# Kernel tuning notes

Hardware: AMD Instinct MI355X
Metric: run time of the kernel (lower is better)

## Reference

```python
import jax, jax.numpy as jnp
import numpy as np

E = 128      # embedding_dim
H = 64       # hidden_dim
B = 2048     # batch
L = 200      # history length
NEG = -1e30  # stand-in for -inf (avoids NaN for all-pad rows; same math when any key unmasked)


def setup_inputs() -> dict:
    key = jax.random.key(0)
    ks = jax.random.split(key, 10)
    s1 = 1.0 / np.sqrt(4 * E)
    s2 = 1.0 / np.sqrt(H)
    return {
        "query": jax.random.normal(ks[0], (B, E), jnp.float32),
        "keys": jax.random.normal(ks[1], (B, L, E), jnp.float32),
        "mask": jax.random.randint(ks[2], (B, L), 0, 2, jnp.int32),
        "W1": jax.random.uniform(ks[3], (4 * E, H), jnp.float32, -s1, s1),
        "b1": jax.random.uniform(ks[4], (H,), jnp.float32, -s1, s1),
        "W2": jax.random.uniform(ks[5], (H, H), jnp.float32, -s2, s2),
        "b2": jax.random.uniform(ks[6], (H,), jnp.float32, -s2, s2),
        "W3": jax.random.uniform(ks[7], (H, 1), jnp.float32, -s2, s2),
        "b3": jax.random.uniform(ks[8], (1,), jnp.float32, -s2, s2),
        "no_hist": jax.random.normal(ks[9], (E,), jnp.float32) * 0.001,
    }


def reference(query, keys, mask, W1, b1, W2, b2, W3, b3, no_hist):
    # q expanded over L, 4-way concat features: [q, k, q*k, q-k] -> (B, L, 4E)
    q = jnp.broadcast_to(query[:, None, :], keys.shape)
    attn_in = jnp.concatenate([q, keys, q * keys, q - keys], axis=-1)
    # 3-layer MLP scorer -> (B, L)
    h = jax.nn.relu(attn_in @ W1 + b1)
    h = jax.nn.relu(h @ W2 + b2)
    scores = (h @ W3 + b3)[..., 0]
    # masked softmax over L, then zero masked slots and renormalize
    m = mask.astype(scores.dtype)
    scores = jnp.where(m == 0, NEG, scores)
    attn = jax.nn.softmax(scores, axis=1) * m
    denom = jnp.sum(attn, axis=1, keepdims=True)
    attn = attn / (denom + 1e-12)
    # weighted sum of keys -> (B, E)
    user_interest = jnp.einsum("bl,ble->be", attn, keys)
    # rows with no history get the learned no-hist embedding
    all_pad = jnp.sum(m, axis=1) == 0  # (B,)
    user_interest = jnp.where(all_pad[:, None], no_hist[None, :], user_interest)
    return user_interest
```

## Files before the change

kernel.cpp:

```cpp
#include <hip/hip_runtime.h>


#define NB 2048
#define LE 128
#define LH 64
#define LL 200

typedef short bf16x8 __attribute__((ext_vector_type(8)));
typedef float f32x4 __attribute__((ext_vector_type(4)));

__device__ float g_BD[8192];
__device__ float g_Cq[8192];
__device__ float g_AD[8192];
__device__ short g_W2T[4096];

__device__ __forceinline__ short f2bf(float f) {
  unsigned u = __float_as_uint(f);
  u += 0x7fffu + ((u >> 16) & 1u);
  return (short)(u >> 16);
}

__device__ __forceinline__ unsigned cvtpk(float a, float b) {
  unsigned d;
  asm("v_cvt_pk_bf16_f32 %0, %1, %2" : "=v"(d) : "v"(a), "v"(b));
  return d;
}

__global__ void k0_prep(const float* __restrict__ W1, const float* __restrict__ W2) {
  int idx = blockIdx.x * 256 + threadIdx.x;
  if (idx < 8192) {
    int h = idx >> 7, e = idx & 127;
    g_BD[idx] = W1[(128 + e) * LH + h] - W1[(384 + e) * LH + h];
    g_Cq[idx] = W1[(256 + e) * LH + h];
    int e2 = idx >> 6, h2 = idx & 63;
    g_AD[idx] = W1[e2 * LH + h2] + W1[(384 + e2) * LH + h2];
    if (idx < 4096) {
      int c = idx >> 6, k = idx & 63;
      g_W2T[idx] = f2bf(W2[k * LH + c]);
    }
  }
}

struct __align__(16) SM {
  short flds1[16 * 64 * 8];
  short flds2[8 * 64 * 8];
  short h1[4][16 * 68];
  float scores[208];
  float q[128];
  float bias1[64];
  float b2s[64];
  float w3s[64];
  float red[16];
  float redf[512];
};

__global__ void __launch_bounds__(256, 4)
din_attn(const float* __restrict__ query, const float* __restrict__ keysg,
         const int* __restrict__ mask, const float* __restrict__ b1,
         const float* __restrict__ b2, const float* __restrict__ W3,
         const float* __restrict__ no_hist, float* __restrict__ out)
{
  __shared__ SM sm;
  const int b    = blockIdx.x;
  const int t    = threadIdx.x;
  const int lane = t & 63;
  const int wv   = t >> 6;
  const int col  = lane & 15;
  const int quad = lane >> 4;

  int my_mask = 0;
  if (t < LL) my_mask = mask[b * LL + t];
  if (t < LE) sm.q[t] = query[b * LE + t];
  if (t < LH) { sm.b2s[t] = b2[t]; sm.w3s[t] = W3[t]; }
  __syncthreads();

  #pragma unroll
  for (int i = 0; i < 4; ++i) {
    int idx = (t + 256 * i) * 8;
    int h = idx >> 7, e0 = idx & 127;
    float4 bd0 = *(const float4*)&g_BD[idx];
    float4 bd1 = *(const float4*)&g_BD[idx + 4];
    float4 c0  = *(const float4*)&g_Cq[idx];
    float4 c1  = *(const float4*)&g_Cq[idx + 4];
    int4 w;
    w.x = (int)cvtpk(bd0.x + sm.q[e0 + 0] * c0.x, bd0.y + sm.q[e0 + 1] * c0.y);
    w.y = (int)cvtpk(bd0.z + sm.q[e0 + 2] * c0.z, bd0.w + sm.q[e0 + 3] * c0.w);
    w.z = (int)cvtpk(bd1.x + sm.q[e0 + 4] * c1.x, bd1.y + sm.q[e0 + 5] * c1.y);
    w.w = (int)cvtpk(bd1.z + sm.q[e0 + 6] * c1.z, bd1.w + sm.q[e0 + 7] * c1.w);
    int n = h >> 4, cc = h & 15, kt = e0 >> 5, qd = (e0 >> 3) & 3;
    *(int4*)&sm.flds1[(((n * 4 + kt) * 64) + qd * 16 + cc) * 8] = w;
  }
  {
    int l = t & 63, f0 = t >> 6;
    #pragma unroll
    for (int ii = 0; ii < 2; ++ii) {
      int f = f0 + ii * 4;
      int n = f >> 1, k2 = f & 1;
      int cc = l & 15, qd = l >> 4;
      *(bf16x8*)&sm.flds2[(f * 64 + l) * 8] =
          *(const bf16x8*)&g_W2T[(n * 16 + cc) * 64 + k2 * 32 + qd * 8];
    }
  }
  {
    int h = lane;
    float acc = 0.f;
    #pragma unroll 8
    for (int e = wv * 32; e < wv * 32 + 32; ++e)
      acc = fmaf(sm.q[e], g_AD[e * LH + h], acc);
    float* biasp = (float*)&sm.h1[0][0];
    biasp[wv * 64 + h] = acc;
  }
  __syncthreads();

  if (t < LH) {
    const float* biasp = (const float*)&sm.h1[0][0];
    sm.bias1[t] = b1[t] + biasp[t] + biasp[64 + t] + biasp[128 + t] + biasp[192 + t];
  }
  __syncthreads();

  const float* kb = keysg + (size_t)b * LL * LE;
  short* h1w = &sm.h1[wv][0];
  const int mts[4] = {wv, wv + 4, wv + 8, 12};
  bf16x8 ka[4][4];

  auto load_tile = [&](bf16x8 (&a)[4], int mt) {
    int row = mt * 16 + col;
    row = row < LL ? row : LL - 1;
    const float* rp = kb + row * LE;
    #pragma unroll
    for (int kt = 0; kt < 4; ++kt) {
      float4 v0 = *(const float4*)&rp[kt * 32 + quad * 8];
      float4 v1 = *(const float4*)&rp[kt * 32 + quad * 8 + 4];
      int4 w;
      w.x = (int)cvtpk(v0.x, v0.y);
      w.y = (int)cvtpk(v0.z, v0.w);
      w.z = (int)cvtpk(v1.x, v1.y);
      w.w = (int)cvtpk(v1.z, v1.w);
      a[kt] = *(bf16x8*)&w;
    }
  };

  auto compute_tile = [&](const bf16x8 (&a)[4], int mt) {
    #pragma unroll
    for (int n = 0; n < 4; ++n) {
      f32x4 acc = {0.f, 0.f, 0.f, 0.f};
      #pragma unroll
      for (int kt = 0; kt < 4; ++kt) {
        bf16x8 wf = *(const bf16x8*)&sm.flds1[((n * 4 + kt) * 64 + lane) * 8];
        acc = __builtin_amdgcn_mfma_f32_16x16x32_bf16(wf, a[kt], acc, 0, 0, 0);
      }
      float4 bb = *(const float4*)&sm.bias1[n * 16 + quad * 4];
      int2 wr;
      wr.x = (int)cvtpk(fmaxf(acc[0] + bb.x, 0.f), fmaxf(acc[1] + bb.y, 0.f));
      wr.y = (int)cvtpk(fmaxf(acc[2] + bb.z, 0.f), fmaxf(acc[3] + bb.w, 0.f));
      *(int2*)&h1w[col * 68 + n * 16 + quad * 4] = wr;
    }
    bf16x8 a2[2];
    #pragma unroll
    for (int k2 = 0; k2 < 2; ++k2)
      a2[k2] = *(const bf16x8*)&h1w[col * 68 + k2 * 32 + quad * 8];
    float p[4] = {0.f, 0.f, 0.f, 0.f};
    #pragma unroll
    for (int n = 0; n < 4; ++n) {
      bf16x8 w20 = *(const bf16x8*)&sm.flds2[((n * 2 + 0) * 64 + lane) * 8];
      bf16x8 w21 = *(const bf16x8*)&sm.flds2[((n * 2 + 1) * 64 + lane) * 8];
      f32x4 c2 = {0.f, 0.f, 0.f, 0.f};
      c2 = __builtin_amdgcn_mfma_f32_16x16x32_bf16(a2[0], w20, c2, 0, 0, 0);
      c2 = __builtin_amdgcn_mfma_f32_16x16x32_bf16(a2[1], w21, c2, 0, 0, 0);
      float bb = sm.b2s[n * 16 + col];
      float w3 = sm.w3s[n * 16 + col];
      #pragma unroll
      for (int j = 0; j < 4; ++j)
        p[j] = fmaf(fmaxf(c2[j] + bb, 0.f), w3, p[j]);
    }
    {
      bool s8 = (col & 8) != 0;
      float k0 = s8 ? p[2] : p[0], d0 = s8 ? p[0] : p[2];
      float k1 = s8 ? p[3] : p[1], d1 = s8 ? p[1] : p[3];
      k0 += __shfl_xor(d0, 8);
      k1 += __shfl_xor(d1, 8);
      bool s4 = (col & 4) != 0;
      float u = s4 ? k1 : k0, du = s4 ? k0 : k1;
      u += __shfl_xor(du, 4);
      u += __shfl_xor(u, 2);
      u += __shfl_xor(u, 1);
      if ((col & 3) == 0) sm.scores[mt * 16 + quad * 4 + (col >> 2)] = u;
    }
  };

  load_tile(ka[0], mts[0]);
  load_tile(ka[1], mts[1]);
  compute_tile(ka[0], mts[0]);
  load_tile(ka[2], mts[2]);
  compute_tile(ka[1], mts[1]);
  if (wv == 0) load_tile(ka[3], 12);
  compute_tile(ka[2], mts[2]);
  if (wv == 0) compute_tile(ka[3], 12);
  __syncthreads();

  float sc = (t < LL) ? sm.scores[t] : -3.0e38f;
  float vmax = (my_mask != 0) ? sc : -3.0e38f;
  #pragma unroll
  for (int off = 1; off < 64; off <<= 1) vmax = fmaxf(vmax, __shfl_xor(vmax, off));
  if (lane == 0) sm.red[wv] = vmax;
  __syncthreads();
  float M = fmaxf(fmaxf(sm.red[0], sm.red[1]), fmaxf(sm.red[2], sm.red[3]));
  float ex = (t < LL && my_mask != 0) ? __expf(sc - M) : 0.f;
  float vsum = ex;
  #pragma unroll
  for (int off = 1; off < 64; off <<= 1) vsum += __shfl_xor(vsum, off);
  if (lane == 0) sm.red[4 + wv] = vsum;
  __syncthreads();
  float Z = sm.red[4] + sm.red[5] + sm.red[6] + sm.red[7];
  bool allpad = !(Z > 0.f);
  float rz = allpad ? 0.f : (1.f / Z);
  if (t < 208) sm.scores[t] = (t < LL) ? ex * rz : 0.f;
  __syncthreads();

  {
    const int nt = (wv == 0) ? 4 : 3;
    float v[32];
    #pragma unroll
    for (int k = 0; k < 32; ++k) v[k] = 0.f;
    #pragma unroll
    for (int i = 0; i < 4; ++i) {
      if (i < nt) {
        float aw = sm.scores[mts[i] * 16 + col];
        #pragma unroll
        for (int kt = 0; kt < 4; ++kt) {
          const int* kv = (const int*)&ka[i][kt];
          #pragma unroll
          for (int w = 0; w < 4; ++w) {
            unsigned u = (unsigned)kv[w];
            v[kt * 8 + 2 * w]     = fmaf(aw, __uint_as_float(u << 16), v[kt * 8 + 2 * w]);
            v[kt * 8 + 2 * w + 1] = fmaf(aw, __uint_as_float(u & 0xffff0000u), v[kt * 8 + 2 * w + 1]);
          }
        }
      }
    }
    #pragma unroll
    for (int step = 0; step < 4; ++step) {
      const int off  = 8 >> step;
      const int half = 16 >> step;
      bool sel = (col & off) != 0;
      #pragma unroll
      for (int k = 0; k < 16; ++k) {
        if (k < half) {
          float keep = sel ? v[k + half] : v[k];
          float send = sel ? v[k] : v[k + half];
          v[k] = keep + __shfl_xor(send, off);
        }
      }
    }
    int e0 = (col >> 2) * 32 + quad * 8 + ((col & 3) * 2);
    *(float2*)&sm.redf[wv * 128 + e0] = make_float2(v[0], v[1]);
    __syncthreads();
    if (t < LE) {
      float s = sm.redf[t] + sm.redf[128 + t] + sm.redf[256 + t] + sm.redf[384 + t];
      if (allpad) s = no_hist[t];
      out[b * LE + t] = s;
    }
  }
}

extern "C" void kernel_launch(void* const* d_in, const int* in_sizes, int n_in,
                              void* d_out, int out_size, void* d_ws, size_t ws_size,
                              hipStream_t stream) {
  (void)in_sizes; (void)n_in; (void)ws_size; (void)out_size; (void)d_ws;
  const float* query   = (const float*)d_in[0];
  const float* keysg   = (const float*)d_in[1];
  const int*   mask    = (const int*)d_in[2];
  const float* W1      = (const float*)d_in[3];
  const float* b1      = (const float*)d_in[4];
  const float* W2      = (const float*)d_in[5];
  const float* b2      = (const float*)d_in[6];
  const float* W3      = (const float*)d_in[7];
  const float* no_hist = (const float*)d_in[9];

  k0_prep<<<32, 256, 0, stream>>>(W1, W2);
  din_attn<<<NB, 256, 0, stream>>>(query, keysg, mask, b1, b2, W3, no_hist,
                                   (float*)d_out);
}
```

Before: 313.5 us.

## Process two batch rows per block and prefetch first key tile early

The kernel now launches 1024 blocks that each loop over two batch rows, so per-block setup (W2 fragment staging, b2/W3 loads) is amortized. For each row, the first key tile's raw float loads are issued before the per-query weight folding and bias computation, overlapping that global latency with setup work. The softmax normalization is folded into the weighted-sum weights, which removes one barrier and the rescale write pass. Halving the grid risks lower latency hiding if fewer resident blocks cannot cover the memory traffic. The early prefetch also raises register pressure.

```diff
diff --git a/kernel.cpp b/kernel.cpp
--- a/kernel.cpp
+++ b/kernel.cpp
@@ -61,35 +61,16 @@
          const float* __restrict__ no_hist, float* __restrict__ out)
 {
   __shared__ SM sm;
-  const int b    = blockIdx.x;
   const int t    = threadIdx.x;
   const int lane = t & 63;
   const int wv   = t >> 6;
   const int col  = lane & 15;
   const int quad = lane >> 4;
-
-  int my_mask = 0;
-  if (t < LL) my_mask = mask[b * LL + t];
-  if (t < LE) sm.q[t] = query[b * LE + t];
+  const int mts[4] = {wv, wv + 4, wv + 8, 12};
+  const int nt = (wv == 0) ? 4 : 3;
+  short* h1w = &sm.h1[wv][0];
+
   if (t < LH) { sm.b2s[t] = b2[t]; sm.w3s[t] = W3[t]; }
-  __syncthreads();
-
-  #pragma unroll
-  for (int i = 0; i < 4; ++i) {
-    int idx = (t + 256 * i) * 8;
-    int h = idx >> 7, e0 = idx & 127;
-    float4 bd0 = *(const float4*)&g_BD[idx];
-    float4 bd1 = *(const float4*)&g_BD[idx + 4];
-    float4 c0  = *(const float4*)&g_Cq[idx];
-    float4 c1  = *(const float4*)&g_Cq[idx + 4];
-    int4 w;
-    w.x = (int)cvtpk(bd0.x + sm.q[e0 + 0] * c0.x, bd0.y + sm.q[e0 + 1] * c0.y);
-    w.y = (int)cvtpk(bd0.z + sm.q[e0 + 2] * c0.z, bd0.w + sm.q[e0 + 3] * c0.w);
-    w.z = (int)cvtpk(bd1.x + sm.q[e0 + 4] * c1.x, bd1.y + sm.q[e0 + 5] * c1.y);
-    w.w = (int)cvtpk(bd1.z + sm.q[e0 + 6] * c1.z, bd1.w + sm.q[e0 + 7] * c1.w);
-    int n = h >> 4, cc = h & 15, kt = e0 >> 5, qd = (e0 >> 3) & 3;
-    *(int4*)&sm.flds1[(((n * 4 + kt) * 64) + qd * 16 + cc) * 8] = w;
-  }
   {
     int l = t & 63, f0 = t >> 6;
     #pragma unroll
@@ -101,29 +82,8 @@
           *(const bf16x8*)&g_W2T[(n * 16 + cc) * 64 + k2 * 32 + qd * 8];
     }
   }
-  {
-    int h = lane;
-    float acc = 0.f;
-    #pragma unroll 8
-    for (int e = wv * 32; e < wv * 32 + 32; ++e)
-      acc = fmaf(sm.q[e], g_AD[e * LH + h], acc);
-    float* biasp = (float*)&sm.h1[0][0];
-    biasp[wv * 64 + h] = acc;
-  }
-  __syncthreads();
-
-  if (t < LH) {
-    const float* biasp = (const float*)&sm.h1[0][0];
-    sm.bias1[t] = b1[t] + biasp[t] + biasp[64 + t] + biasp[128 + t] + biasp[192 + t];
-  }
-  __syncthreads();
-
-  const float* kb = keysg + (size_t)b * LL * LE;
-  short* h1w = &sm.h1[wv][0];
-  const int mts[4] = {wv, wv + 4, wv + 8, 12};
-  bf16x8 ka[4][4];
-
-  auto load_tile = [&](bf16x8 (&a)[4], int mt) {
+
+  auto load_tile = [&](bf16x8 (&a)[4], const float* kb, int mt) {
     int row = mt * 16 + col;
     row = row < LL ? row : LL - 1;
     const float* rp = kb + row * LE;
@@ -188,77 +148,140 @@
     }
   };
 
-  load_tile(ka[0], mts[0]);
-  load_tile(ka[1], mts[1]);
-  compute_tile(ka[0], mts[0]);
-  load_tile(ka[2], mts[2]);
-  compute_tile(ka[1], mts[1]);
-  if (wv == 0) load_tile(ka[3], 12);
-  compute_tile(ka[2], mts[2]);
-  if (wv == 0) compute_tile(ka[3], 12);
-  __syncthreads();
-
-  float sc = (t < LL) ? sm.scores[t] : -3.0e38f;
-  float vmax = (my_mask != 0) ? sc : -3.0e38f;
-  #pragma unroll
-  for (int off = 1; off < 64; off <<= 1) vmax = fmaxf(vmax, __shfl_xor(vmax, off));
-  if (lane == 0) sm.red[wv] = vmax;
-  __syncthreads();
-  float M = fmaxf(fmaxf(sm.red[0], sm.red[1]), fmaxf(sm.red[2], sm.red[3]));
-  float ex = (t < LL && my_mask != 0) ? __expf(sc - M) : 0.f;
-  float vsum = ex;
-  #pragma unroll
-  for (int off = 1; off < 64; off <<= 1) vsum += __shfl_xor(vsum, off);
-  if (lane == 0) sm.red[4 + wv] = vsum;
-  __syncthreads();
-  float Z = sm.red[4] + sm.red[5] + sm.red[6] + sm.red[7];
-  bool allpad = !(Z > 0.f);
-  float rz = allpad ? 0.f : (1.f / Z);
-  if (t < 208) sm.scores[t] = (t < LL) ? ex * rz : 0.f;
-  __syncthreads();
-
-  {
-    const int nt = (wv == 0) ? 4 : 3;
-    float v[32];
-    #pragma unroll
-    for (int k = 0; k < 32; ++k) v[k] = 0.f;
+  #pragma unroll 1
+  for (int r = 0; r < 2; ++r) {
+    const int b = blockIdx.x + (r << 10);
+    const float* kb = keysg + (size_t)b * LL * LE;
+
+    float4 r0[8];
+    {
+      const float* rp = kb + (mts[0] * 16 + col) * LE;
+      #pragma unroll
+      for (int kt = 0; kt < 4; ++kt) {
+        r0[2 * kt]     = *(const float4*)&rp[kt * 32 + quad * 8];
+        r0[2 * kt + 1] = *(const float4*)&rp[kt * 32 + quad * 8 + 4];
+      }
+    }
+
+    int my_mask = 0;
+    if (t < LL) my_mask = mask[b * LL + t];
+    if (t < LE) sm.q[t] = query[b * LE + t];
+    __syncthreads();
+
     #pragma unroll
     for (int i = 0; i < 4; ++i) {
-      if (i < nt) {
-        float aw = sm.scores[mts[i] * 16 + col];
-        #pragma unroll
-        for (int kt = 0; kt < 4; ++kt) {
-          const int* kv = (const int*)&ka[i][kt];
+      int idx = (t + 256 * i) * 8;
+      int h = idx >> 7, e0 = idx & 127;
+      float4 bd0 = *(const float4*)&g_BD[idx];
+      float4 bd1 = *(const float4*)&g_BD[idx + 4];
+      float4 c0  = *(const float4*)&g_Cq[idx];
+      float4 c1  = *(const float4*)&g_Cq[idx + 4];
+      int4 w;
+      w.x = (int)cvtpk(bd0.x + sm.q[e0 + 0] * c0.x, bd0.y + sm.q[e0 + 1] * c0.y);
+      w.y = (int)cvtpk(bd0.z + sm.q[e0 + 2] * c0.z, bd0.w + sm.q[e0 + 3] * c0.w);
+      w.z = (int)cvtpk(bd1.x + sm.q[e0 + 4] * c1.x, bd1.y + sm.q[e0 + 5] * c1.y);
+      w.w = (int)cvtpk(bd1.z + sm.q[e0 + 6] * c1.z, bd1.w + sm.q[e0 + 7] * c1.w);
+      int n = h >> 4, cc = h & 15, kt = e0 >> 5, qd = (e0 >> 3) & 3;
+      *(int4*)&sm.flds1[(((n * 4 + kt) * 64) + qd * 16 + cc) * 8] = w;
+    }
+    {
+      int h = lane;
+      float acc = 0.f;
+      #pragma unroll 8
+      for (int e = wv * 32; e < wv * 32 + 32; ++e)
+        acc = fmaf(sm.q[e], g_AD[e * LH + h], acc);
+      float* biasp = (float*)&sm.h1[0][0];
+      biasp[wv * 64 + h] = acc;
+    }
+    __syncthreads();
+
+    if (t < LH) {
+      const float* biasp = (const float*)&sm.h1[0][0];
+      sm.bias1[t] = b1[t] + biasp[t] + biasp[64 + t] + biasp[128 + t] + biasp[192 + t];
+    }
+    __syncthreads();
+
+    bf16x8 ka[4][4];
+    {
+      #pragma unroll
+      for (int kt = 0; kt < 4; ++kt) {
+        int4 w;
+        w.x = (int)cvtpk(r0[2 * kt].x, r0[2 * kt].y);
+        w.y = (int)cvtpk(r0[2 * kt].z, r0[2 * kt].w);
+        w.z = (int)cvtpk(r0[2 * kt + 1].x, r0[2 * kt + 1].y);
+        w.w = (int)cvtpk(r0[2 * kt + 1].z, r0[2 * kt + 1].w);
+        ka[0][kt] = *(bf16x8*)&w;
+      }
+    }
+    load_tile(ka[1], kb, mts[1]);
+    compute_tile(ka[0], mts[0]);
+    load_tile(ka[2], kb, mts[2]);
+    compute_tile(ka[1], mts[1]);
+    if (wv == 0) load_tile(ka[3], kb, 12);
+    compute_tile(ka[2], mts[2]);
+    if (wv == 0) compute_tile(ka[3], 12);
+    __syncthreads();
+
+    float sc = (t < LL) ? sm.scores[t] : -3.0e38f;
+    float vmax = (my_mask != 0) ? sc : -3.0e38f;
+    #pragma unroll
+    for (int off = 1; off < 64; off <<= 1) vmax = fmaxf(vmax, __shfl_xor(vmax, off));
+    if (lane == 0) sm.red[wv] = vmax;
+    __syncthreads();
+    float M = fmaxf(fmaxf(sm.red[0], sm.red[1]), fmaxf(sm.red[2], sm.red[3]));
+    float ex = (t < LL && my_mask != 0) ? __expf(sc - M) : 0.f;
+    if (t < 208) sm.scores[t] = (t < LL) ? ex : 0.f;
+    float vsum = ex;
+    #pragma unroll
+    for (int off = 1; off < 64; off <<= 1) vsum += __shfl_xor(vsum, off);
+    if (lane == 0) sm.red[4 + wv] = vsum;
+    __syncthreads();
+    float Z = sm.red[4] + sm.red[5] + sm.red[6] + sm.red[7];
+    bool allpad = !(Z > 0.f);
+    float rz = allpad ? 0.f : (1.f / Z);
+
+    {
+      float v[32];
+      #pragma unroll
+      for (int k = 0; k < 32; ++k) v[k] = 0.f;
+      #pragma unroll
+      for (int i = 0; i < 4; ++i) {
+        if (i < nt) {
+          float aw = sm.scores[mts[i] * 16 + col] * rz;
           #pragma unroll
-          for (int w = 0; w < 4; ++w) {
-            unsigned u = (unsigned)kv[w];
-            v[kt * 8 + 2 * w]     = fmaf(aw, __uint_as_float(u << 16), v[kt * 8 + 2 * w]);
-            v[kt * 8 + 2 * w + 1] = fmaf(aw, __uint_as_float(u & 0xffff0000u), v[kt * 8 + 2 * w + 1]);
+          for (int kt = 0; kt < 4; ++kt) {
+            const int* kv = (const int*)&ka[i][kt];
+            #pragma unroll
+            for (int w = 0; w < 4; ++w) {
+              unsigned u = (unsigned)kv[w];
+              v[kt * 8 + 2 * w]     = fmaf(aw, __uint_as_float(u << 16), v[kt * 8 + 2 * w]);
+              v[kt * 8 + 2 * w + 1] = fmaf(aw, __uint_as_float(u & 0xffff0000u), v[kt * 8 + 2 * w + 1]);
+            }
           }
         }
       }
-    }
-    #pragma unroll
-    for (int step = 0; step < 4; ++step) {
-      const int off  = 8 >> step;
-      const int half = 16 >> step;
-      bool sel = (col & off) != 0;
-      #pragma unroll
-      for (int k = 0; k < 16; ++k) {
-        if (k < half) {
-          float keep = sel ? v[k + half] : v[k];
-          float send = sel ? v[k] : v[k + half];
-          v[k] = keep + __shfl_xor(send, off);
+      #pragma unroll
+      for (int step = 0; step < 4; ++step) {
+        const int off  = 8 >> step;
+        const int half = 16 >> step;
+        bool sel = (col & off) != 0;
+        #pragma unroll
+        for (int k = 0; k < 16; ++k) {
+          if (k < half) {
+            float keep = sel ? v[k + half] : v[k];
+            float send = sel ? v[k] : v[k + half];
+            v[k] = keep + __shfl_xor(send, off);
+          }
         }
       }
-    }
-    int e0 = (col >> 2) * 32 + quad * 8 + ((col & 3) * 2);
-    *(float2*)&sm.redf[wv * 128 + e0] = make_float2(v[0], v[1]);
-    __syncthreads();
-    if (t < LE) {
-      float s = sm.redf[t] + sm.redf[128 + t] + sm.redf[256 + t] + sm.redf[384 + t];
-      if (allpad) s = no_hist[t];
-      out[b * LE + t] = s;
+      int e0 = (col >> 2) * 32 + quad * 8 + ((col & 3) * 2);
+      *(float2*)&sm.redf[wv * 128 + e0] = make_float2(v[0], v[1]);
+      __syncthreads();
+      if (t < LE) {
+        float s = sm.redf[t] + sm.redf[128 + t] + sm.redf[256 + t] + sm.redf[384 + t];
+        if (allpad) s = no_hist[t];
+        out[b * LE + t] = s;
+      }
     }
   }
 }
@@ -278,6 +301,6 @@
   const float* no_hist = (const float*)d_in[9];
 
   k0_prep<<<32, 256, 0, stream>>>(W1, W2);
-  din_attn<<<NB, 256, 0, stream>>>(query, keysg, mask, b1, b2, W3, no_hist,
-                                   (float*)d_out);
-}
+  din_attn<<<1024, 256, 0, stream>>>(query, keysg, mask, b1, b2, W3, no_hist,
+                                     (float*)d_out);
+}
```

Measured after the change: 350.9 us. 1.12x slower.
